# Performance work log

Measured on AMD Instinct MI355X. Metric: run time of the kernel, lower is better.

The kernel has to match this reference:

```python
import jax, jax.numpy as jnp
import numpy as np

B, T, D_MODEL, HEAD_DIM = 4, 4096, 1024, 2


def setup_inputs() -> dict:
    key = jax.random.key(0)
    kx, kq, kk, kv = jax.random.split(key, 4)
    x = jax.random.normal(kx, (B, T, D_MODEL), dtype=jnp.float32)
    # nn.Linear weights: (out_features, in_features), applied as x @ W.T
    s_qk = 1.0 / np.sqrt(D_MODEL)
    W_Q = jax.random.uniform(kq, (HEAD_DIM, D_MODEL), minval=-s_qk, maxval=s_qk, dtype=jnp.float32)
    W_K = jax.random.uniform(kk, (HEAD_DIM, D_MODEL), minval=-s_qk, maxval=s_qk, dtype=jnp.float32)
    W_V = jax.random.uniform(kv, (D_MODEL, D_MODEL), minval=-s_qk, maxval=s_qk, dtype=jnp.float32)
    # strict upper-triangular True = masked (future positions)
    causal_mask = jnp.triu(jnp.ones((T, T), dtype=bool), k=1)[None, :, :]
    return {"x": x, "W_Q": W_Q, "W_K": W_K, "W_V": W_V, "causal_mask": causal_mask}


def reference(x, W_Q, W_K, W_V, causal_mask):
    # x: (B, T, d_model)
    Q = jnp.einsum('btd,hd->bth', x, W_Q)   # (B, T, head_dim)
    K = jnp.einsum('bsd,hd->bsh', x, W_K)   # (B, S, head_dim)
    V = jnp.einsum('bsd,ed->bse', x, W_V)   # (B, S, d_model)
    scores = jnp.einsum('bth,bsh->bts', Q, K)              # (B, T, S)
    scores = jnp.where(causal_mask, -jnp.inf, scores)
    max_idx = jnp.argmax(scores, axis=-1)                  # (B, T)
    # one-hot scatter + bmm in the original == hard gather of V rows
    out = jnp.take_along_axis(V, max_idx[..., None], axis=1)  # (B, T, d_model)
    return out
```

## Files before the change

kernel.cpp:

```cpp
#include <hip/hip_runtime.h>
#include <math.h>

#define TT 4096
#define DM 1024
#define BB 4
#define BT (BB * TT)
#define SENT  0x7f7f7f7f
#define MAGIC 0x17C3A5E9


__device__ __forceinline__ float dot4(const float4 a, const float4 b) {
    return a.x * b.x + a.y * b.y + a.z * b.z + a.w * b.w;
}
__device__ __forceinline__ int aload(const int* p) {
    return __hip_atomic_load((int*)p, __ATOMIC_RELAXED, __HIP_MEMORY_SCOPE_AGENT);
}
__device__ __forceinline__ void astore(int* p, int v) {
    __hip_atomic_store(p, v, __ATOMIC_RELAXED, __HIP_MEMORY_SCOPE_AGENT);
}
__device__ __forceinline__ void astore64(unsigned long long* p, unsigned long long v) {
    __hip_atomic_store(p, v, __ATOMIC_RELAXED, __HIP_MEMORY_SCOPE_AGENT);
}
__device__ __forceinline__ unsigned long long packf2(float a, float b) {
    union { float2 f; unsigned long long u; } cv;
    cv.f = make_float2(a, b);
    return cv.u;
}
__device__ __forceinline__ void spin_eq(const int* p, int v) {
    int it = 0;
    while (__hip_atomic_load((int*)p, __ATOMIC_RELAXED, __HIP_MEMORY_SCOPE_AGENT) != v) {
        __builtin_amdgcn_s_sleep(8);
        if (++it > (1 << 21)) break;
    }
}

__global__ __launch_bounds__(256, 4) void qk_am_kernel(
    const float* __restrict__ x, const float* __restrict__ wq,
    const float* __restrict__ wk,
    unsigned long long* __restrict__ Qu, unsigned long long* __restrict__ Ku,
    int* __restrict__ idx, int* __restrict__ rep, int* __restrict__ rowdone,
    int* __restrict__ chunkdone, const int* __restrict__ gen)
{
    __shared__ union {
        float4 w[4][256];
        float2 ks[TT];
    } sm;

    const int tid  = threadIdx.x;
    const int bid  = blockIdx.x;
    const int wave = tid >> 6, lane = tid & 63;

    const int expv = MAGIC ^ aload(gen);

    if (bid < 512) {
        sm.w[0][tid] = ((const float4*)(wq))[tid];
        sm.w[1][tid] = ((const float4*)(wq + DM))[tid];
        sm.w[2][tid] = ((const float4*)(wk))[tid];
        sm.w[3][tid] = ((const float4*)(wk + DM))[tid];
        if (tid < 32) {
            const int rg = bid * 32 + tid;
            astore(&rep[rg], SENT);
            astore(&idx[rg], -1);
            astore(&rowdone[rg], 0);
        }
        __syncthreads();

        #pragma unroll
        for (int rr = 0; rr < 8; ++rr) {
            const int row = bid * 32 + wave * 8 + rr;
            const float4* xr = (const float4*)(x + (size_t)row * DM);
            float s0 = 0.f, s1 = 0.f, s2 = 0.f, s3 = 0.f;
            #pragma unroll
            for (int j = 0; j < 4; ++j) {
                const float4 xv = xr[j * 64 + lane];
                s0 += dot4(xv, sm.w[0][j * 64 + lane]);
                s1 += dot4(xv, sm.w[1][j * 64 + lane]);
                s2 += dot4(xv, sm.w[2][j * 64 + lane]);
                s3 += dot4(xv, sm.w[3][j * 64 + lane]);
            }
            #pragma unroll
            for (int off = 32; off > 0; off >>= 1) {
                s0 += __shfl_down(s0, off);
                s1 += __shfl_down(s1, off);
                s2 += __shfl_down(s2, off);
                s3 += __shfl_down(s3, off);
            }
            if (lane == 0) {
                astore64(&Qu[row], packf2(s0, s1));
                astore64(&Ku[row], packf2(s2, s3));
            }
        }
        __syncthreads();
        if (tid == 0) astore(&chunkdone[bid], expv);
    }

    const float* Kf = (const float*)Ku;
    const float* Qf = (const float*)Qu;
    for (int pp = 0; pp < 2; ++pp) {
        const int p = bid * 2 + pp;
        const int b = p >> 9, j = p & 511;
        const int cmax = ((1023 - j) * 4 + 3) >> 5;
        if (tid <= cmax) spin_eq(&chunkdone[b * 128 + tid], expv);
        __syncthreads();

        const int nfill4 = (((1023 - j) * 4 + 4) >> 1);
        const float4* kb4 = (const float4*)(Kf + (size_t)b * TT * 2);
        float4* ks4 = (float4*)sm.ks;
        for (int i = tid; i < nfill4; i += 256) ks4[i] = kb4[i];
        __syncthreads();

        const float4* kp = (const float4*)sm.ks;
        #pragma unroll
        for (int u = 0; u < 2; ++u) {
            const int tg = u ? j : (1023 - j);
            const int t = tg * 4 + wave;
            const float2 q = ((const float2*)Qf)[b * TT + t];

            float best = -INFINITY;
            int bi = 0x7fffffff;
            int pq = lane;
            while (2 * (pq + 64) + 1 <= t) {
                const float4 a = kp[pq];
                const float4 c = kp[pq + 64];
                const float c0 = q.x * a.x + q.y * a.y;
                const float c1 = q.x * a.z + q.y * a.w;
                const float c2 = q.x * c.x + q.y * c.y;
                const float c3 = q.x * c.z + q.y * c.w;
                if (c0 > best) { best = c0; bi = 2 * pq; }
                if (c1 > best) { best = c1; bi = 2 * pq + 1; }
                if (c2 > best) { best = c2; bi = 2 * (pq + 64); }
                if (c3 > best) { best = c3; bi = 2 * (pq + 64) + 1; }
                pq += 128;
            }
            while (2 * pq <= t) {
                const float4 a = kp[pq];
                const float c0 = q.x * a.x + q.y * a.y;
                if (c0 > best) { best = c0; bi = 2 * pq; }
                if (2 * pq + 1 <= t) {
                    const float c1 = q.x * a.z + q.y * a.w;
                    if (c1 > best) { best = c1; bi = 2 * pq + 1; }
                }
                pq += 64;
            }
            #pragma unroll
            for (int off = 32; off > 0; off >>= 1) {
                const float ov = __shfl_down(best, off);
                const int   oi = __shfl_down(bi, off);
                if (ov > best || (ov == best && oi < bi)) { best = ov; bi = oi; }
            }
            if (lane == 0) {
                astore(&idx[b * TT + t], bi);
                atomicMin(&rep[b * TT + bi], t);
            }
        }
        __syncthreads();
    }
}

__global__ __launch_bounds__(256, 4) void vrow_gather_kernel(
    const float* __restrict__ x, const float* __restrict__ wv,
    const int* __restrict__ idx, const int* __restrict__ rep,
    int* __restrict__ rowdone, int* __restrict__ gen,
    float* __restrict__ out)
{
    __shared__ int hits_n;
    __shared__ int hits_g[4096];

    const int tid  = threadIdx.x;
    const int bid  = blockIdx.x;
    const int wave = tid >> 6, lane = tid & 63;

    const int slice = bid >> 4;
    const int usub  = bid & 15;
    const int e0 = slice * 16 + wave * 4;
    float4 w[4][4];
    #pragma unroll
    for (int r = 0; r < 4; ++r) {
        const float4* wr = (const float4*)(wv + (size_t)(e0 + r) * DM);
        #pragma unroll
        for (int jj = 0; jj < 4; ++jj) w[r][jj] = wr[jj * 64 + lane];
    }
    if (tid == 0) hits_n = 0;
    __syncthreads();
    #pragma unroll
    for (int k = 0; k < 4; ++k) {
        const int m4 = tid + 256 * k;
        const int g = usub + (m4 << 4);
        const int s = aload(&idx[g]);
        const int b2 = g >> 12;
        if (aload(&rep[(b2 << 12) + s]) == (g & (TT - 1))) {
            const int pos = atomicAdd(&hits_n, 1);
            hits_g[pos] = g;
        }
    }
    __syncthreads();
    const int nh = hits_n;
    for (int h = 0; h < nh; ++h) {
        const int g  = hits_g[h];
        const int b2 = g >> 12;
        const int s  = aload(&idx[g]);
        const int bs = (b2 << 12) + s;
        const float4* xr = (const float4*)(x + (size_t)bs * DM);
        float4 xv[4];
        #pragma unroll
        for (int jj = 0; jj < 4; ++jj) xv[jj] = xr[jj * 64 + lane];
        float s0 = 0.f, s1 = 0.f, s2 = 0.f, s3 = 0.f;
        #pragma unroll
        for (int jj = 0; jj < 4; ++jj) {
            s0 += dot4(w[0][jj], xv[jj]);
            s1 += dot4(w[1][jj], xv[jj]);
            s2 += dot4(w[2][jj], xv[jj]);
            s3 += dot4(w[3][jj], xv[jj]);
        }
        #pragma unroll
        for (int off = 32; off > 0; off >>= 1) {
            s0 += __shfl_down(s0, off);
            s1 += __shfl_down(s1, off);
            s2 += __shfl_down(s2, off);
            s3 += __shfl_down(s3, off);
        }
        if (lane == 0) {
            unsigned long long* op = (unsigned long long*)(out + (size_t)g * DM + e0);
            astore64(op,     packf2(s0, s1));
            astore64(op + 1, packf2(s2, s3));
        }
        __syncthreads();
        if (tid == 0) atomicAdd(&rowdone[bs], 1);
    }

    for (int r4 = 0; r4 < 4; ++r4) {
        const int g  = bid * 16 + r4 * 4 + wave;
        const int b2 = g >> 12, tl = g & (TT - 1);
        const int s  = aload(&idx[g]);
        const int bs = (b2 << 12) + s;
        const int r  = aload(&rep[bs]);
        if (r == tl) continue;
        int it = 0;
        while (aload(&rowdone[bs]) != 64) {
            __builtin_amdgcn_s_sleep(8);
            if (++it > (1 << 21)) break;
        }
        asm volatile("" ::: "memory");
        const float4* src = (const float4*)(out + ((size_t)(b2 * TT + r)) * DM);
        float4* dst = (float4*)(out + (size_t)g * DM);
        #pragma unroll
        for (int k2 = 0; k2 < 4; ++k2) dst[k2 * 64 + lane] = src[k2 * 64 + lane];
    }

    __syncthreads();
    if (bid == 0 && tid == 0) atomicAdd(gen, 1);
}

extern "C" void kernel_launch(void* const* d_in, const int* in_sizes, int n_in,
                              void* d_out, int out_size, void* d_ws, size_t ws_size,
                              hipStream_t stream) {
    const float* x  = (const float*)d_in[0];
    const float* wq = (const float*)d_in[1];
    const float* wk = (const float*)d_in[2];
    const float* wv = (const float*)d_in[3];
    float* out = (float*)d_out;

    char* ws = (char*)d_ws;
    unsigned long long* Qu = (unsigned long long*)(ws);
    unsigned long long* Ku = (unsigned long long*)(ws + 131072);
    int* idx       = (int*)(ws + 262144);
    int* rep       = (int*)(ws + 327680);
    int* rowdone   = (int*)(ws + 393216);
    int* chunkdone = (int*)(ws + 458752);
    int* gen       = (int*)(ws + 460800);

    qk_am_kernel<<<1024, 256, 0, stream>>>(x, wq, wk, Qu, Ku,
                                           idx, rep, rowdone, chunkdone, gen);
    vrow_gather_kernel<<<1024, 256, 0, stream>>>(x, wv, idx, rep,
                                                 rowdone, gen, out);
}
```

Measured before the change: 229.2 us.

## Split V-row compute and duplicate-row gather into separate kernels

Replaces the in-kernel spin-wait on per-row completion counters with a third kernel launch that copies duplicated output rows after all representative rows are computed. This removes the atomic rowdone counters, the block-wide barriers per hit row and the busy-wait loops, and lets plain loads and one float4 store replace relaxed atomics. In exchange it adds a kernel launch boundary and loses overlap between computing rows and copying duplicates.

```diff
diff --git a/kernel.cpp b/kernel.cpp
--- a/kernel.cpp
+++ b/kernel.cpp
@@ -157,10 +157,9 @@
     }
 }
 
-__global__ __launch_bounds__(256, 4) void vrow_gather_kernel(
+__global__ __launch_bounds__(256, 4) void vrow_kernel(
     const float* __restrict__ x, const float* __restrict__ wv,
     const int* __restrict__ idx, const int* __restrict__ rep,
-    int* __restrict__ rowdone, int* __restrict__ gen,
     float* __restrict__ out)
 {
     __shared__ int hits_n;
@@ -186,9 +185,9 @@
     for (int k = 0; k < 4; ++k) {
         const int m4 = tid + 256 * k;
         const int g = usub + (m4 << 4);
-        const int s = aload(&idx[g]);
+        const int s = idx[g];
         const int b2 = g >> 12;
-        if (aload(&rep[(b2 << 12) + s]) == (g & (TT - 1))) {
+        if (rep[(b2 << 12) + s] == (g & (TT - 1))) {
             const int pos = atomicAdd(&hits_n, 1);
             hits_g[pos] = g;
         }
@@ -198,7 +197,7 @@
     for (int h = 0; h < nh; ++h) {
         const int g  = hits_g[h];
         const int b2 = g >> 12;
-        const int s  = aload(&idx[g]);
+        const int s  = idx[g];
         const int bs = (b2 << 12) + s;
         const float4* xr = (const float4*)(x + (size_t)bs * DM);
         float4 xv[4];
@@ -219,36 +218,26 @@
             s2 += __shfl_down(s2, off);
             s3 += __shfl_down(s3, off);
         }
-        if (lane == 0) {
-            unsigned long long* op = (unsigned long long*)(out + (size_t)g * DM + e0);
-            astore64(op,     packf2(s0, s1));
-            astore64(op + 1, packf2(s2, s3));
-        }
-        __syncthreads();
-        if (tid == 0) atomicAdd(&rowdone[bs], 1);
-    }
-
-    for (int r4 = 0; r4 < 4; ++r4) {
-        const int g  = bid * 16 + r4 * 4 + wave;
-        const int b2 = g >> 12, tl = g & (TT - 1);
-        const int s  = aload(&idx[g]);
-        const int bs = (b2 << 12) + s;
-        const int r  = aload(&rep[bs]);
-        if (r == tl) continue;
-        int it = 0;
-        while (aload(&rowdone[bs]) != 64) {
-            __builtin_amdgcn_s_sleep(8);
-            if (++it > (1 << 21)) break;
-        }
-        asm volatile("" ::: "memory");
-        const float4* src = (const float4*)(out + ((size_t)(b2 * TT + r)) * DM);
-        float4* dst = (float4*)(out + (size_t)g * DM);
-        #pragma unroll
-        for (int k2 = 0; k2 < 4; ++k2) dst[k2 * 64 + lane] = src[k2 * 64 + lane];
-    }
-
-    __syncthreads();
-    if (bid == 0 && tid == 0) atomicAdd(gen, 1);
+        if (lane == 0)
+            *(float4*)(out + (size_t)g * DM + e0) = make_float4(s0, s1, s2, s3);
+    }
+}
+
+__global__ __launch_bounds__(256) void gather_kernel(const int* __restrict__ idx,
+                                                     const int* __restrict__ rep,
+                                                     int* __restrict__ gen,
+                                                     float* __restrict__ out) {
+    const int tid = threadIdx.x, wave = tid >> 6, lane = tid & 63;
+    const int bt = blockIdx.x * 4 + wave;
+    const int b = bt >> 12, t = bt & (TT - 1);
+    const int s = idx[bt];
+    const int r = rep[b * TT + s];
+    if (blockIdx.x == 0 && tid == 0) atomicAdd(gen, 1);
+    if (r == t) return;
+    const float4* src = (const float4*)(out + ((size_t)(b * TT + r)) * DM);
+    float4* dst = (float4*)(out + (size_t)bt * DM);
+    #pragma unroll
+    for (int k = 0; k < 4; ++k) dst[k * 64 + lane] = src[k * 64 + lane];
 }
 
 extern "C" void kernel_launch(void* const* d_in, const int* in_sizes, int n_in,
@@ -271,6 +260,6 @@
 
     qk_am_kernel<<<1024, 256, 0, stream>>>(x, wq, wk, Qu, Ku,
                                            idx, rep, rowdone, chunkdone, gen);
-    vrow_gather_kernel<<<1024, 256, 0, stream>>>(x, wv, idx, rep,
-                                                 rowdone, gen, out);
-}
+    vrow_kernel<<<1024, 256, 0, stream>>>(x, wv, idx, rep, out);
+    gather_kernel<<<BT / 4, 256, 0, stream>>>(idx, rep, gen, out);
+}
```

Result: faster. 217.5 us (-5.1%).
